# Optimization experiments

Measured on AMD Instinct MI355X. Metric: run time of the kernel, lower is better.

Reference implementation:

```python
import jax, jax.numpy as jnp
import numpy as np

N_EMB = 4096
EMB_DIM = 256
BETA = 10.0


def setup_inputs() -> dict:
    key = jax.random.key(0)
    k1, k2 = jax.random.split(key)
    z = jax.random.normal(k1, (32, EMB_DIM, 32, 32), dtype=jnp.float32)
    # matches nn.Embedding init: uniform(-1/n_embeddings, 1/n_embeddings)
    embedding = jax.random.uniform(
        k2, (N_EMB, EMB_DIM), dtype=jnp.float32,
        minval=-1.0 / N_EMB, maxval=1.0 / N_EMB)
    return {"z": z, "embedding": embedding}


def reference(z, embedding):
    sg = jax.lax.stop_gradient
    # NCHW -> NHWC
    zp = jnp.transpose(z, (0, 2, 3, 1))  # [B,H,W,D]
    zf = zp.reshape(-1, EMB_DIM)         # [N,D]
    # squared distances: ||z||^2 + ||e||^2 - 2 z.e^T
    d = (jnp.sum(zf * zf, axis=1, keepdims=True)
         + jnp.sum(embedding * embedding, axis=1)
         - 2.0 * jnp.matmul(zf, embedding.T))  # [N,K]
    min_encoding_indices = jnp.argmin(d, axis=1)  # [N]
    z_q = embedding[min_encoding_indices].reshape(zp.shape)  # [B,H,W,D]
    loss = (jnp.mean((sg(z_q) - zp) ** 2)
            + BETA * jnp.mean((z_q - sg(zp)) ** 2))
    # straight-through estimator
    z_q_ste = zp + sg(z_q - zp)
    z_q_out = jnp.transpose(z_q_ste, (0, 3, 1, 2))  # back to NCHW
    return (z_q_out, loss, min_encoding_indices)
```

## Files before the change

kernel.cpp:

```cpp
#include <hip/hip_runtime.h>

#define DIM   256
#define HW_   1024
#define NROWS 32768
#define KEMB  4096

#define WS_S_OFF    131072
#define WS_E_OFF    262144
#define WS_LOSS_OFF 278528
#define WS_DONE_OFF 278536
#define WS_CNT_OFF  278592
#define WS_CAND_OFF 540736
#define WS_EBUF_OFF 1589312
#define WS_NEEDED   3686464
#define RESCUE_W    1.5e-4f

typedef __attribute__((ext_vector_type(8))) short bf16x8;
typedef __attribute__((ext_vector_type(4))) float f32x4;

__device__ __forceinline__ unsigned short f2bf(float v) {
  unsigned u = __float_as_uint(v);
  return (unsigned short)((u + 0x7FFFu + ((u >> 16) & 1u)) >> 16);
}

__device__ __forceinline__ float np_sumsq_128(const float* q, int stride) {
#pragma clang fp contract(off)
  float r[8];
#pragma unroll
  for (int i = 0; i < 8; ++i) { float v = q[i * stride]; r[i] = v * v; }
  for (int blk = 8; blk < 128; blk += 8) {
#pragma unroll
    for (int i = 0; i < 8; ++i) {
      float v = q[(blk + i) * stride];
      float sq = v * v;
      r[i] = r[i] + sq;
    }
  }
  return ((r[0] + r[1]) + (r[2] + r[3])) + ((r[4] + r[5]) + (r[6] + r[7]));
}

__global__ __launch_bounds__(256) void prep_kernel(
    const float* __restrict__ z, const float* __restrict__ emb,
    float* __restrict__ S, float* __restrict__ E, short* __restrict__ ebuf,
    double* __restrict__ loss_sum, int* __restrict__ done, int do_filter) {
#pragma clang fp contract(off)
  if (blockIdx.x < 144) {
    int t = blockIdx.x * 256 + threadIdx.x;
    if (t == 0) { loss_sum[0] = 0.0; done[0] = 0; }
    if (t < NROWS) {
      if (!do_filter) {
        int b = t >> 10, hw = t & 1023;
        const float* p = z + (size_t)b * (DIM * HW_) + hw;
        float s0 = np_sumsq_128(p, HW_);
        float s1 = np_sumsq_128(p + 128 * HW_, HW_);
        S[t] = s0 + s1;
      }
    } else if (t < NROWS + KEMB) {
      int j = t - NROWS;
      const float* p = emb + (size_t)j * DIM;
      float s0 = np_sumsq_128(p, 1);
      float s1 = np_sumsq_128(p + 128, 1);
      E[j] = s0 + s1;
    }
  } else {
    if (!do_filter) return;
    int u = (blockIdx.x - 144) * 256 + threadIdx.x;
    int lane = u & 63;
    int ks = (u >> 6) & 7;
    int g16 = u >> 9;
    int j = g16 * 16 + (lane & 15);
    int kb = ks * 32 + (lane >> 4) * 8;
    const float* p = emb + (size_t)j * DIM + kb;
    short out[8];
#pragma unroll
    for (int i = 0; i < 8; ++i) out[i] = (short)f2bf(p[i]);
    *(bf16x8*)(ebuf + (size_t)u * 8) = *(bf16x8*)out;
  }
}

__global__ __launch_bounds__(512, 3) void filter2_kernel(
    const float* __restrict__ z, const short* __restrict__ ebuf,
    const float* __restrict__ E, int* __restrict__ cnt_g,
    int* __restrict__ cand_g) {
  __shared__ __align__(16) short Ab[32 * 512];
  __shared__ float rowmin_l[64][8];
  __shared__ float thr_l[64];
  __shared__ int   cnt_l[64];
  __shared__ int   cand_l[64][8];

  const int t = threadIdx.x;
  const int w = t >> 6, lane = t & 63;
  const int quad = lane >> 4, l16 = lane & 15;
  const int nb = blockIdx.x * 64;
  const int b = nb >> 10, hwb = nb & 1023;

  {
    const float* zb2 = z + (size_t)b * (DIM * HW_) + hwb;
    const int k0 = w * 32 + quad * 8;
#pragma unroll
    for (int mt = 0; mt < 4; ++mt) {
      const int r = mt * 16 + l16;
      short tmp[8];
#pragma unroll
      for (int i = 0; i < 8; ++i)
        tmp[i] = (short)f2bf(zb2[(size_t)(k0 + i) * HW_ + r]);
      *(bf16x8*)(Ab + ((mt * 8 + w) * 64 + lane) * 8) = *(bf16x8*)tmp;
    }
  }
  __syncthreads();

  const f32x4 zero = {0.0f, 0.0f, 0.0f, 0.0f};
  const short* Abl = Ab + lane * 8;

  float runmin[4][4];
#pragma unroll
  for (int mt = 0; mt < 4; ++mt)
#pragma unroll
    for (int rg = 0; rg < 4; ++rg) runmin[mt][rg] = 3.0e38f;

#pragma unroll 1
  for (int grp = 0; grp < 8; ++grp) {
    const int jb = w * 512 + grp * 64;
    const int g16b = jb >> 4;
    f32x4 acc[4][4];
#pragma unroll
    for (int jt = 0; jt < 4; ++jt)
#pragma unroll
      for (int mt = 0; mt < 4; ++mt) acc[jt][mt] = zero;
#pragma unroll 1
    for (int ks = 0; ks < 8; ++ks) {
      bf16x8 av[4];
#pragma unroll
      for (int mt = 0; mt < 4; ++mt)
        av[mt] = *(const bf16x8*)(Abl + (mt * 8 + ks) * 512);
#pragma unroll
      for (int jt = 0; jt < 4; ++jt) {
        bf16x8 bfr = *(const bf16x8*)(ebuf +
            ((size_t)(g16b + jt) * 8 + ks) * 512 + lane * 8);
#pragma unroll
        for (int mt = 0; mt < 4; ++mt)
          acc[jt][mt] = __builtin_amdgcn_mfma_f32_16x16x32_bf16(
              av[mt], bfr, acc[jt][mt], 0, 0, 0);
      }
    }
#pragma unroll
    for (int jt = 0; jt < 4; ++jt) {
      float Ej = E[jb + jt * 16 + l16];
#pragma unroll
      for (int mt = 0; mt < 4; ++mt)
#pragma unroll
        for (int rg = 0; rg < 4; ++rg) {
          float g = fmaf(-2.0f, acc[jt][mt][rg], Ej);
          runmin[mt][rg] = fminf(runmin[mt][rg], g);
        }
    }
  }
#pragma unroll
  for (int mt = 0; mt < 4; ++mt)
#pragma unroll
    for (int rg = 0; rg < 4; ++rg) {
      float m = runmin[mt][rg];
#pragma unroll
      for (int mask = 1; mask <= 8; mask <<= 1)
        m = fminf(m, __shfl_xor(m, mask, 64));
      runmin[mt][rg] = m;
    }
  if (l16 == 0) {
#pragma unroll
    for (int mt = 0; mt < 4; ++mt)
#pragma unroll
      for (int rg = 0; rg < 4; ++rg)
        rowmin_l[mt * 16 + quad * 4 + rg][w] = runmin[mt][rg];
  }
  __syncthreads();
  if (t < 64) {
    float m0 = fminf(fminf(rowmin_l[t][0], rowmin_l[t][1]),
                     fminf(rowmin_l[t][2], rowmin_l[t][3]));
    float m1 = fminf(fminf(rowmin_l[t][4], rowmin_l[t][5]),
                     fminf(rowmin_l[t][6], rowmin_l[t][7]));
    thr_l[t] = fminf(m0, m1) + RESCUE_W;
    cnt_l[t] = 0;
  }
  __syncthreads();
  float thrv[4][4];
#pragma unroll
  for (int mt = 0; mt < 4; ++mt)
#pragma unroll
    for (int rg = 0; rg < 4; ++rg)
      thrv[mt][rg] = thr_l[mt * 16 + quad * 4 + rg];

#pragma unroll 1
  for (int grp = 0; grp < 8; ++grp) {
    const int jb = w * 512 + grp * 64;
    const int g16b = jb >> 4;
    f32x4 acc[4][4];
#pragma unroll
    for (int jt = 0; jt < 4; ++jt)
#pragma unroll
      for (int mt = 0; mt < 4; ++mt) acc[jt][mt] = zero;
#pragma unroll 1
    for (int ks = 0; ks < 8; ++ks) {
      bf16x8 av[4];
#pragma unroll
      for (int mt = 0; mt < 4; ++mt)
        av[mt] = *(const bf16x8*)(Abl + (mt * 8 + ks) * 512);
#pragma unroll
      for (int jt = 0; jt < 4; ++jt) {
        bf16x8 bfr = *(const bf16x8*)(ebuf +
            ((size_t)(g16b + jt) * 8 + ks) * 512 + lane * 8);
#pragma unroll
        for (int mt = 0; mt < 4; ++mt)
          acc[jt][mt] = __builtin_amdgcn_mfma_f32_16x16x32_bf16(
              av[mt], bfr, acc[jt][mt], 0, 0, 0);
      }
    }
#pragma unroll
    for (int jt = 0; jt < 4; ++jt) {
      int jcol = jb + jt * 16 + l16;
      float Ej = E[jcol];
#pragma unroll
      for (int mt = 0; mt < 4; ++mt)
#pragma unroll
        for (int rg = 0; rg < 4; ++rg) {
          float g = fmaf(-2.0f, acc[jt][mt][rg], Ej);
          if (g <= thrv[mt][rg]) {
            int rl = mt * 16 + quad * 4 + rg;
            int slot = atomicAdd(&cnt_l[rl], 1);
            if (slot < 8) cand_l[rl][slot] = jcol;
          }
        }
    }
  }
  __syncthreads();
  if (t < 64) {
    int c = cnt_l[t];
    cnt_g[nb + t] = c;
    int cc = c > 8 ? 8 : c;
    for (int p = 0; p < cc; ++p) cand_g[(size_t)(nb + t) * 8 + p] = cand_l[t][p];
  }
}

#define XPAD 257
__global__ __launch_bounds__(256, 2) void exact_cand_kernel(
    const float* __restrict__ z, const float* __restrict__ emb,
    const float* __restrict__ E,
    const int* __restrict__ cnt_g, const int* __restrict__ cand_g,
    int* __restrict__ idx_out, float* __restrict__ idxf_out) {
#pragma clang fp contract(off)
  __shared__ float z_l[64 * XPAD];
  const int t = threadIdx.x;
  const int nb = blockIdx.x * 64;
  const int b = nb >> 10, hwb = nb & 1023;
  const float* zb = z + (size_t)b * (DIM * HW_) + hwb;
#pragma unroll
  for (int i = 0; i < 16; ++i) {
    int flat = i * 256 + t;
    int d = flat >> 4, r4 = flat & 15;
    float4 v = *(const float4*)(zb + (size_t)d * HW_ + r4 * 4);
    z_l[(r4 * 4 + 0) * XPAD + d] = v.x;
    z_l[(r4 * 4 + 1) * XPAD + d] = v.y;
    z_l[(r4 * 4 + 2) * XPAD + d] = v.z;
    z_l[(r4 * 4 + 3) * XPAD + d] = v.w;
  }
  __syncthreads();

  const int r = t >> 2, p = t & 3;
  const int row = nb + r;
  const float* zrow = z_l + r * XPAD;
  float s;
  {
    float s0 = np_sumsq_128(zrow, 1);
    float s1 = np_sumsq_128(zrow + 128, 1);
    s = s0 + s1;
  }
  int c = cnt_g[row];
  float bd = 3.0e38f; int bj = 0x7fffffff;
  if (c <= 8) {
    for (int q = p; q < c; q += 4) {
      int j = cand_g[(size_t)row * 8 + q];
      const float* e = emb + (size_t)j * DIM;
      float acc = 0.0f;
#pragma unroll 8
      for (int k4 = 0; k4 < 64; ++k4) {
        float4 ev = *(const float4*)(e + k4 * 4);
        acc = fmaf(zrow[k4 * 4 + 0], ev.x, acc);
        acc = fmaf(zrow[k4 * 4 + 1], ev.y, acc);
        acc = fmaf(zrow[k4 * 4 + 2], ev.z, acc);
        acc = fmaf(zrow[k4 * 4 + 3], ev.w, acc);
      }
      float d = fmaf(-2.0f, acc, s + E[j]);
      if (d < bd || (d == bd && j < bj)) { bd = d; bj = j; }
    }
  } else if (p == 0) {
    for (int j = 0; j < KEMB; ++j) {
      const float* e = emb + (size_t)j * DIM;
      float acc = 0.0f;
      for (int k4 = 0; k4 < 64; ++k4) {
        float4 ev = *(const float4*)(e + k4 * 4);
        acc = fmaf(zrow[k4 * 4 + 0], ev.x, acc);
        acc = fmaf(zrow[k4 * 4 + 1], ev.y, acc);
        acc = fmaf(zrow[k4 * 4 + 2], ev.z, acc);
        acc = fmaf(zrow[k4 * 4 + 3], ev.w, acc);
      }
      float d = fmaf(-2.0f, acc, s + E[j]);
      if (d < bd || (d == bd && j < bj)) { bd = d; bj = j; }
    }
  }
#pragma unroll
  for (int m = 1; m <= 2; m <<= 1) {
    float od = __shfl_xor(bd, m, 64);
    int   oj = __shfl_xor(bj, m, 64);
    if (od < bd || (od == bd && oj < bj)) { bd = od; bj = oj; }
  }
  if (p == 0) { idx_out[row] = bj; idxf_out[row] = (float)bj; }
}

#define RT 64
#define JT 256
#define KC 16
__global__ __launch_bounds__(256, 2) void dist_argmin_kernel(
    const float* __restrict__ z, const float* __restrict__ emb,
    const float* __restrict__ S, const float* __restrict__ E,
    int* __restrict__ idx_out, float* __restrict__ idxf_out) {
  __shared__ float zt[DIM * RT];
  __shared__ float et[KC * JT];
  const int t  = threadIdx.x;
  const int g  = t & 31;
  const int tr = t >> 5;
  const int nb = blockIdx.x * RT;
  const int b  = nb >> 10;
  const int hwb = nb & 1023;
  const float* zb = z + (size_t)b * (DIM * HW_) + hwb;
#pragma unroll
  for (int i = 0; i < 16; ++i) {
    int flat = t + i * 256;
    int k  = flat >> 4;
    int r4 = flat & 15;
    float4 v = *(const float4*)(zb + (size_t)k * HW_ + r4 * 4);
    *(float4*)(zt + flat * 4) = v;
  }
  float bestd[8];
  int   bestj[8];
#pragma unroll
  for (int i = 0; i < 8; ++i) { bestd[i] = 3.0e38f; bestj[i] = 0; }
  float Sreg[8];
#pragma unroll
  for (int rr = 0; rr < 8; ++rr) Sreg[rr] = S[nb + tr * 8 + rr];
  float4 pf[4];
#pragma unroll
  for (int q = 0; q < 4; ++q) {
    int cid = q * 256 + t;
    pf[q] = *(const float4*)(emb + (size_t)(cid >> 2) * DIM + (cid & 3) * 4);
  }
  for (int jt = 0; jt < KEMB / JT; ++jt) {
    float acc[8][8];
#pragma unroll
    for (int rr = 0; rr < 8; ++rr)
#pragma unroll
      for (int c = 0; c < 8; ++c) acc[rr][c] = 0.0f;
    for (int kc = 0; kc < DIM / KC; ++kc) {
      __syncthreads();
#pragma unroll
      for (int q = 0; q < 4; ++q) {
        int cid = q * 256 + t;
        int j = cid >> 2, k4 = cid & 3;
        et[(k4 * 4 + 0) * JT + j] = pf[q].x;
        et[(k4 * 4 + 1) * JT + j] = pf[q].y;
        et[(k4 * 4 + 2) * JT + j] = pf[q].z;
        et[(k4 * 4 + 3) * JT + j] = pf[q].w;
      }
      int s = jt * (DIM / KC) + kc + 1;
      if (s < (KEMB / JT) * (DIM / KC)) {
        int njt = s >> 4, nkc = s & 15;
        const float* base = emb + (size_t)njt * JT * DIM + nkc * KC;
#pragma unroll
        for (int q = 0; q < 4; ++q) {
          int cid = q * 256 + t;
          pf[q] = *(const float4*)(base + (size_t)(cid >> 2) * DIM + (cid & 3) * 4);
        }
      }
      __syncthreads();
      const float* ztk = zt + (kc * KC) * RT;
#pragma unroll
      for (int kk = 0; kk < KC; ++kk) {
        float4 z0 = *(const float4*)(ztk + kk * RT + tr * 8);
        float4 z1 = *(const float4*)(ztk + kk * RT + tr * 8 + 4);
        float2 e0 = *(const float2*)(et + kk * JT + g * 2);
        float2 e1 = *(const float2*)(et + kk * JT + 64 + g * 2);
        float2 e2 = *(const float2*)(et + kk * JT + 128 + g * 2);
        float2 e3 = *(const float2*)(et + kk * JT + 192 + g * 2);
        float zr[8] = {z0.x, z0.y, z0.z, z0.w, z1.x, z1.y, z1.z, z1.w};
        float ev[8] = {e0.x, e0.y, e1.x, e1.y, e2.x, e2.y, e3.x, e3.y};
#pragma unroll
        for (int rr = 0; rr < 8; ++rr)
#pragma unroll
          for (int c = 0; c < 8; ++c)
            acc[rr][c] = fmaf(zr[rr], ev[c], acc[rr][c]);
      }
    }
    int jb = jt * JT;
    float Ereg[8];
#pragma unroll
    for (int c = 0; c < 8; ++c)
      Ereg[c] = E[jb + (c >> 1) * 64 + g * 2 + (c & 1)];
#pragma unroll
    for (int rr = 0; rr < 8; ++rr)
#pragma unroll
      for (int c = 0; c < 8; ++c) {
        float A = Sreg[rr] + Ereg[c];
        float d = fmaf(-2.0f, acc[rr][c], A);
        int j = jb + (c >> 1) * 64 + g * 2 + (c & 1);
        if (d < bestd[rr] || (d == bestd[rr] && j < bestj[rr])) {
          bestd[rr] = d; bestj[rr] = j;
        }
      }
  }
  __syncthreads();
  float* rd = et;
  int*   rj = (int*)(et + 2048);
#pragma unroll
  for (int rr = 0; rr < 8; ++rr) {
    rd[(tr * 8 + rr) * 32 + g] = bestd[rr];
    rj[(tr * 8 + rr) * 32 + g] = bestj[rr];
  }
  __syncthreads();
  if (t < RT) {
    float bd = rd[t * 32];
    int   bj = rj[t * 32];
    for (int c = 1; c < 32; ++c) {
      float d2 = rd[t * 32 + c];
      int   j2 = rj[t * 32 + c];
      if (d2 < bd || (d2 == bd && j2 < bj)) { bd = d2; bj = j2; }
    }
    idx_out[nb + t]  = bj;
    idxf_out[nb + t] = (float)bj;
  }
}

#define EPAD 257
__global__ __launch_bounds__(256) void epilogue_kernel(
    const float* __restrict__ z, const float* __restrict__ emb,
    const int* __restrict__ idx, float* __restrict__ out0,
    double* __restrict__ loss_sum, int* __restrict__ done,
    float* __restrict__ out_loss) {
#pragma clang fp contract(off)
  __shared__ float eq[64 * EPAD];
  __shared__ int   iv_l[64];
  __shared__ double wsum[4];
  const int t = threadIdx.x, w = t >> 6, lane = t & 63;
  const int nb = blockIdx.x * 64;
  const int b = nb >> 10, hwb = nb & 1023;

  if (t < 64) iv_l[t] = idx[nb + t];
  __syncthreads();
  const float4* emb4 = (const float4*)emb;
#pragma unroll
  for (int i = 0; i < 16; ++i) {
    int r = w * 16 + i;
    float4 v = emb4[(size_t)iv_l[r] * 64 + lane];
    *(float4*)(eq + r * EPAD + lane * 4) = v;
  }
  __syncthreads();

  double acc = 0.0;
  const float* zb = z + (size_t)b * (DIM * HW_) + hwb;
  float* ob = out0 + (size_t)b * (DIM * HW_) + hwb;
  for (int dc = 0; dc < 64; ++dc) {
    int d = dc * 4 + w;
    float zp = zb[(size_t)d * HW_ + lane];
    float zq = eq[lane * EPAD + d];
    float td = zq - zp;
    ob[(size_t)d * HW_ + lane] = zp + td;
    acc += (double)(td * td);
  }
#pragma unroll
  for (int off = 32; off > 0; off >>= 1) acc += __shfl_down(acc, off, 64);
  if (lane == 0) wsum[w] = acc;
  __syncthreads();
  if (t == 0) {
    double bsum = (wsum[0] + wsum[1]) + (wsum[2] + wsum[3]);
    atomicAdd(loss_sum, bsum);
    __threadfence();
    int prev = atomicAdd(done, 1);
    if (prev == 511) {
      double m = loss_sum[0] / 8388608.0;
      float mf = (float)m;
      float bb = 10.0f * mf;
      out_loss[0] = mf + bb;
    }
  }
}

extern "C" void kernel_launch(void* const* d_in, const int* in_sizes, int n_in,
                              void* d_out, int out_size, void* d_ws, size_t ws_size,
                              hipStream_t stream) {
  const float* z   = (const float*)d_in[0];
  const float* emb = (const float*)d_in[1];
  float* out = (float*)d_out;
  char* ws = (char*)d_ws;
  int*      idx  = (int*)ws;
  float*    S    = (float*)(ws + WS_S_OFF);
  float*    E    = (float*)(ws + WS_E_OFF);
  double*   ls   = (double*)(ws + WS_LOSS_OFF);
  int*      done = (int*)(ws + WS_DONE_OFF);
  int*      cnt  = (int*)(ws + WS_CNT_OFF);
  int*      cand = (int*)(ws + WS_CAND_OFF);
  short*    ebuf = (short*)(ws + WS_EBUF_OFF);

  const int do_filter = (ws_size >= (size_t)WS_NEEDED) ? 1 : 0;

  prep_kernel<<<656, 256, 0, stream>>>(z, emb, S, E, ebuf, ls, done, do_filter);

  if (do_filter) {
    filter2_kernel<<<512, 512, 0, stream>>>(z, ebuf, E, cnt, cand);
    exact_cand_kernel<<<512, 256, 0, stream>>>(z, emb, E, cnt, cand, idx,
                                               out + 8388609);
  } else {
    dist_argmin_kernel<<<NROWS / RT, 256, 0, stream>>>(z, emb, S, E, idx,
                                                       out + 8388609);
  }

  epilogue_kernel<<<512, 256, 0, stream>>>(z, emb, idx, out, ls, done,
                                           out + 8388608);
}
```

Before: 254.6 us.

## Fuse filter passes into single GEMM sweep with running-min candidate buffering

The filter kernel previously ran the bf16 MFMA distance GEMM twice: once for each row's minimum and again to collect candidates under the threshold. It now runs one pass that keeps a per-16-lane running minimum and buffers, in shared memory, every code whose score lies within the rescue window of that running minimum, along with its score. A final pass filters the buffered candidates against the true block-wide threshold. This halves the MFMA and embedding-buffer traffic, at the cost of more shared memory (lower occupancy), extra shuffles per group, more atomics, and a fallback flag (count=KEMB) when a row overflows the 64-entry buffer.

```diff
diff --git a/kernel.cpp b/kernel.cpp
--- a/kernel.cpp
+++ b/kernel.cpp
@@ -78,6 +78,7 @@
   }
 }
 
+#define CCAP 64
 __global__ __launch_bounds__(512, 3) void filter2_kernel(
     const float* __restrict__ z, const short* __restrict__ ebuf,
     const float* __restrict__ E, int* __restrict__ cnt_g,
@@ -86,7 +87,8 @@
   __shared__ float rowmin_l[64][8];
   __shared__ float thr_l[64];
   __shared__ int   cnt_l[64];
-  __shared__ int   cand_l[64][8];
+  __shared__ int   cand_l[64][CCAP + 1];
+  __shared__ float gv_l[64][CCAP + 1];
 
   const int t = threadIdx.x;
   const int w = t >> 6, lane = t & 63;
@@ -107,6 +109,7 @@
       *(bf16x8*)(Ab + ((mt * 8 + w) * 64 + lane) * 8) = *(bf16x8*)tmp;
     }
   }
+  if (t < 64) cnt_l[t] = 0;
   __syncthreads();
 
   const f32x4 zero = {0.0f, 0.0f, 0.0f, 0.0f};
@@ -143,28 +146,41 @@
               av[mt], bfr, acc[jt][mt], 0, 0, 0);
       }
     }
+    float Ejv[4];
+#pragma unroll
+    for (int jt = 0; jt < 4; ++jt) Ejv[jt] = E[jb + jt * 16 + l16];
+
+#pragma unroll
+    for (int mt = 0; mt < 4; ++mt)
+#pragma unroll
+      for (int rg = 0; rg < 4; ++rg) {
+        float gm = fmaf(-2.0f, acc[0][mt][rg], Ejv[0]);
+#pragma unroll
+        for (int jt = 1; jt < 4; ++jt)
+          gm = fminf(gm, fmaf(-2.0f, acc[jt][mt][rg], Ejv[jt]));
+#pragma unroll
+        for (int mask = 1; mask <= 8; mask <<= 1)
+          gm = fminf(gm, __shfl_xor(gm, mask, 64));
+        runmin[mt][rg] = fminf(runmin[mt][rg], gm);
+      }
+
 #pragma unroll
     for (int jt = 0; jt < 4; ++jt) {
-      float Ej = E[jb + jt * 16 + l16];
+      int jcol = jb + jt * 16 + l16;
 #pragma unroll
       for (int mt = 0; mt < 4; ++mt)
 #pragma unroll
         for (int rg = 0; rg < 4; ++rg) {
-          float g = fmaf(-2.0f, acc[jt][mt][rg], Ej);
-          runmin[mt][rg] = fminf(runmin[mt][rg], g);
+          float g = fmaf(-2.0f, acc[jt][mt][rg], Ejv[jt]);
+          if (g <= runmin[mt][rg] + RESCUE_W) {
+            int rl = mt * 16 + quad * 4 + rg;
+            int slot = atomicAdd(&cnt_l[rl], 1);
+            if (slot < CCAP) { cand_l[rl][slot] = jcol; gv_l[rl][slot] = g; }
+          }
         }
     }
   }
-#pragma unroll
-  for (int mt = 0; mt < 4; ++mt)
-#pragma unroll
-    for (int rg = 0; rg < 4; ++rg) {
-      float m = runmin[mt][rg];
-#pragma unroll
-      for (int mask = 1; mask <= 8; mask <<= 1)
-        m = fminf(m, __shfl_xor(m, mask, 64));
-      runmin[mt][rg] = m;
-    }
+
   if (l16 == 0) {
 #pragma unroll
     for (int mt = 0; mt < 4; ++mt)
@@ -179,64 +195,24 @@
     float m1 = fminf(fminf(rowmin_l[t][4], rowmin_l[t][5]),
                      fminf(rowmin_l[t][6], rowmin_l[t][7]));
     thr_l[t] = fminf(m0, m1) + RESCUE_W;
-    cnt_l[t] = 0;
-  }
-  __syncthreads();
-  float thrv[4][4];
-#pragma unroll
-  for (int mt = 0; mt < 4; ++mt)
-#pragma unroll
-    for (int rg = 0; rg < 4; ++rg)
-      thrv[mt][rg] = thr_l[mt * 16 + quad * 4 + rg];
-
-#pragma unroll 1
-  for (int grp = 0; grp < 8; ++grp) {
-    const int jb = w * 512 + grp * 64;
-    const int g16b = jb >> 4;
-    f32x4 acc[4][4];
-#pragma unroll
-    for (int jt = 0; jt < 4; ++jt)
-#pragma unroll
-      for (int mt = 0; mt < 4; ++mt) acc[jt][mt] = zero;
-#pragma unroll 1
-    for (int ks = 0; ks < 8; ++ks) {
-      bf16x8 av[4];
-#pragma unroll
-      for (int mt = 0; mt < 4; ++mt)
-        av[mt] = *(const bf16x8*)(Abl + (mt * 8 + ks) * 512);
-#pragma unroll
-      for (int jt = 0; jt < 4; ++jt) {
-        bf16x8 bfr = *(const bf16x8*)(ebuf +
-            ((size_t)(g16b + jt) * 8 + ks) * 512 + lane * 8);
-#pragma unroll
-        for (int mt = 0; mt < 4; ++mt)
-          acc[jt][mt] = __builtin_amdgcn_mfma_f32_16x16x32_bf16(
-              av[mt], bfr, acc[jt][mt], 0, 0, 0);
-      }
-    }
-#pragma unroll
-    for (int jt = 0; jt < 4; ++jt) {
-      int jcol = jb + jt * 16 + l16;
-      float Ej = E[jcol];
-#pragma unroll
-      for (int mt = 0; mt < 4; ++mt)
-#pragma unroll
-        for (int rg = 0; rg < 4; ++rg) {
-          float g = fmaf(-2.0f, acc[jt][mt][rg], Ej);
-          if (g <= thrv[mt][rg]) {
-            int rl = mt * 16 + quad * 4 + rg;
-            int slot = atomicAdd(&cnt_l[rl], 1);
-            if (slot < 8) cand_l[rl][slot] = jcol;
-          }
+  }
+  __syncthreads();
+
+  if (t < 64) {
+    int m = cnt_l[t];
+    float thr = thr_l[t];
+    if (m > CCAP) {
+      cnt_g[nb + t] = KEMB;
+    } else {
+      int sc = 0;
+      for (int q = 0; q < m; ++q) {
+        if (gv_l[t][q] <= thr) {
+          if (sc < 8) cand_g[(size_t)(nb + t) * 8 + sc] = cand_l[t][q];
+          ++sc;
         }
-    }
-  }
-  __syncthreads();
-  if (t < 64) {
-    int c = cnt_l[t];
-    cnt_g[nb + t] = c;
-    int cc = c > 8 ? 8 : c;
-    for (int p = 0; p < cc; ++p) cand_g[(size_t)(nb + t) * 8 + p] = cand_l[t][p];
+      }
+      cnt_g[nb + t] = sc;
+    }
   }
 }
 
```

Measured after the change: 277.6 us. 1.09x slower.
